# Kernel optimization log

Hardware: AMD Instinct MI355X
Metric: run time of the kernel (lower is better)

The kernel has to match this reference:

```python
import jax, jax.numpy as jnp
import numpy as np

MAX_STEPS = 12          # ns = ceil((t1-t0)/0.2) <= ceil(2/0.2) = 10 for unit dirs, unit sphere
BASE_STEP = 0.2
ABSORPTION = 0.1
SCATTERING = 0.1
DENSITY = 6.0
SIGMA = SCATTERING + ABSORPTION + 0.4   # 0.6, used in sample_transparency
BG = jnp.array([0.572, 0.772, 0.921], dtype=jnp.float32)
LIGHT_COLOR = jnp.array([1.3, 0.3, 0.9], dtype=jnp.float32)
RO = jnp.array([0.0, 0.0, 3.0], dtype=jnp.float32)   # hard-coded ray origin in original


def setup_inputs() -> dict:
    key = jax.random.key(0)
    W = H = 1024
    u = jnp.linspace(-0.5, 0.5, W, dtype=jnp.float32)
    v = jnp.linspace(-0.5, 0.5, H, dtype=jnp.float32)
    uu, vv = jnp.meshgrid(u, v, indexing='ij')
    d = jnp.stack([uu, vv, -jnp.ones_like(uu)], axis=-1)          # camera at z=3 looking at origin
    d = d + 0.001 * jax.random.normal(key, d.shape, dtype=jnp.float32)  # randn jitter
    dirs = d / jnp.linalg.norm(d, axis=-1, keepdims=True)          # unit directions -> bounded ns
    scene = jnp.array([[0.0, 0.0, 0.0, 1.0]], dtype=jnp.float32)   # unit sphere at origin
    return {"scene": scene, "dirs": dirs}


def _ray_march(scene, dirs):
    center = scene[0, 0:3]
    radius = scene[0, 3]
    rd = dirs                                      # [W,H,3]
    oc = RO - center                               # [3]
    a = jnp.sum(rd * rd, axis=-1)                  # [W,H]
    b = 2.0 * jnp.sum(rd * oc, axis=-1)
    c = jnp.dot(oc, oc) - radius * radius
    disc = b * b - 4.0 * a * c
    sq = jnp.sqrt(jnp.where(disc > 0, disc, 1.0))  # safe sqrt (masked later)
    x1 = (-b - sq) / (2.0 * a)
    x2 = (-b + sq) / (2.0 * a)
    # flag: disc>=0 and not (x1<0 and x2<0); since x1<=x2 this is x2>=0
    hit = (disc >= 0) & (x2 >= 0)                  # [W,H]
    t0 = jnp.maximum(x1, 0.0)                      # inside -> t0 = 0
    t1 = x2
    seg = t1 - t0
    ns = jnp.ceil(seg / BASE_STEP)                 # [W,H] float step count
    ns_safe = jnp.maximum(ns, 1.0)
    step = seg / ns_safe                           # per-pixel step size
    s = jnp.exp(-SIGMA * step)                     # per-step sample_transparency

    # static march over MAX_STEPS, masked by i < ns
    steps = jnp.arange(MAX_STEPS, dtype=jnp.float32)                 # [K]
    smask = (steps[None, None, :] < ns[..., None]) & hit[..., None]  # [W,H,K]
    t = t1[..., None] - (steps + 0.5) * step[..., None]              # [W,H,K]
    p = RO + t[..., None] * rd[..., None, :]                         # [W,H,K,3] sample points
    pc = p - center
    # light ray: origin p, direction (0,1,0) -> a=1
    lb = 2.0 * pc[..., 1]
    lc = jnp.sum(pc * pc, axis=-1) - radius * radius
    ld = lb * lb - 4.0 * lc
    lsq = jnp.sqrt(jnp.where(ld > 0, ld, 1.0))
    vt1 = (-lb + lsq) / 2.0
    lhit = (ld >= 0) & (vt1 >= 0)
    la = jnp.exp(-DENSITY * (SCATTERING + ABSORPTION) * vt1)         # light attenuation
    acc = jnp.sum(jnp.where(smask & lhit, la, 0.0), axis=-1)         # [W,H]

    # closed form of the original loop:
    #   result = sum_i la_i * light_color * s^(i+1) * scat*dens*step * s^(ns-i)
    #          = light_color * scat*dens*step * s^(ns+1) * sum_i la_i
    transparency = s ** ns
    result = (SCATTERING * DENSITY) * step * (s ** (ns + 1.0)) * acc  # [W,H]
    color_hit = BG * transparency[..., None] + LIGHT_COLOR * result[..., None]
    pixels = jnp.where(hit[..., None], color_hit, BG)                 # [W,H,3]
    return pixels


def reference(scene, dirs):
    return _ray_march(scene, dirs)
```

## Files before the change

kernel.cpp:

```cpp
#include <hip/hip_runtime.h>
#include <math.h>

__device__ __forceinline__ float fmulr(float a, float b) { return __fmul_rn(a, b); }
__device__ __forceinline__ float faddr(float a, float b) { return __fadd_rn(a, b); }
__device__ __forceinline__ float fsubr(float a, float b) { return __fsub_rn(a, b); }

struct Col { float x, y, z; };

__device__ __forceinline__ Col shade1(float rdx, float rdy, float rdz)
{
    const float BGx = 0.572f, BGy = 0.772f, BGz = 0.921f;
    Col out = {BGx, BGy, BGz};

    float a = faddr(faddr(fmulr(rdx, rdx), fmulr(rdy, rdy)), fmulr(rdz, rdz));
    float b = fmulr(2.0f, fmulr(rdz, 3.0f));
    float disc = fsubr(fmulr(b, b), fmulr(fmulr(4.0f, a), 8.0f));
    if (disc < 0.0f) return out;

    float sq = sqrtf(disc > 0.0f ? disc : 1.0f);
    float twoa = fmulr(2.0f, a);
    float x2 = faddr(-b, sq) / twoa;
    if (x2 < 0.0f) return out;
    float x1 = fsubr(-b, sq) / twoa;

    float t0 = fmaxf(x1, 0.0f);
    float t1 = x2;
    float seg = fsubr(t1, t0);
    float ns = ceilf(seg / 0.2f);
    float step = seg / fmaxf(ns, 1.0f);
    int nsi = (int)fminf(ns, 12.0f);

    float acc = 0.0f;
    for (int k = 0; k < nsi; ++k) {
        float t = fsubr(t1, fmulr((float)k + 0.5f, step));
        float pcx = fmulr(t, rdx);
        float pcy = fmulr(t, rdy);
        float pcz = faddr(3.0f, fmulr(t, rdz));
        float lb = fmulr(2.0f, pcy);
        float lc = fsubr(faddr(faddr(fmulr(pcx, pcx), fmulr(pcy, pcy)), fmulr(pcz, pcz)), 1.0f);
        float ld = fsubr(fmulr(lb, lb), fmulr(4.0f, lc));
        if (ld >= 0.0f) {
            float lsq = sqrtf(ld > 0.0f ? ld : 1.0f);
            float vt1 = fmulr(faddr(-lb, lsq), 0.5f);
            if (vt1 >= 0.0f) acc += __expf(-1.2f * vt1);
        }
    }

    float sn  = __expf(-0.6f * (step * ns));
    float sn1 = __expf(-0.6f * (step * (ns + 1.0f)));
    float result = 0.6f * step * sn1 * acc;
    out.x = BGx * sn + 1.3f * result;
    out.y = BGy * sn + 0.3f * result;
    out.z = BGz * sn + 0.9f * result;
    return out;
}

__device__ __forceinline__ Col shadeg(float rdx, float rdy, float rdz,
                                      float cx, float cy, float cz,
                                      float rr, float ocx, float ocy, float ocz,
                                      float cc)
{
    const float BGx = 0.572f, BGy = 0.772f, BGz = 0.921f;
    Col out = {BGx, BGy, BGz};

    float a = faddr(faddr(fmulr(rdx, rdx), fmulr(rdy, rdy)), fmulr(rdz, rdz));
    float b = fmulr(2.0f, faddr(faddr(fmulr(rdx, ocx), fmulr(rdy, ocy)), fmulr(rdz, ocz)));
    float disc = fsubr(fmulr(b, b), fmulr(fmulr(4.0f, a), cc));
    if (disc < 0.0f) return out;

    float sq = sqrtf(disc > 0.0f ? disc : 1.0f);
    float twoa = fmulr(2.0f, a);
    float x2 = faddr(-b, sq) / twoa;
    if (x2 < 0.0f) return out;
    float x1 = fsubr(-b, sq) / twoa;

    float t0 = fmaxf(x1, 0.0f);
    float t1 = x2;
    float seg = fsubr(t1, t0);
    float ns = ceilf(seg / 0.2f);
    float step = seg / fmaxf(ns, 1.0f);
    int nsi = (int)fminf(ns, 12.0f);

    float acc = 0.0f;
    for (int k = 0; k < nsi; ++k) {
        float t = fsubr(t1, fmulr((float)k + 0.5f, step));
        float pcx = fsubr(faddr(0.0f, fmulr(t, rdx)), cx);
        float pcy = fsubr(faddr(0.0f, fmulr(t, rdy)), cy);
        float pcz = fsubr(faddr(3.0f, fmulr(t, rdz)), cz);
        float lb = fmulr(2.0f, pcy);
        float lc = fsubr(faddr(faddr(fmulr(pcx, pcx), fmulr(pcy, pcy)), fmulr(pcz, pcz)), rr);
        float ld = fsubr(fmulr(lb, lb), fmulr(4.0f, lc));
        if (ld >= 0.0f) {
            float lsq = sqrtf(ld > 0.0f ? ld : 1.0f);
            float vt1 = fmulr(faddr(-lb, lsq), 0.5f);
            if (vt1 >= 0.0f) acc += __expf(-1.2f * vt1);
        }
    }

    float sn  = __expf(-0.6f * (step * ns));
    float sn1 = __expf(-0.6f * (step * (ns + 1.0f)));
    float result = 0.6f * step * sn1 * acc;
    out.x = BGx * sn + 1.3f * result;
    out.y = BGy * sn + 0.3f * result;
    out.z = BGz * sn + 0.9f * result;
    return out;
}

__global__ __launch_bounds__(256)
void raymarch_kernel(const float* __restrict__ scene,
                     const float* __restrict__ dirs,
                     float* __restrict__ out,
                     int npix)
{
    int p = blockIdx.x * blockDim.x + threadIdx.x;
    if (p >= npix) return;

    float rdx = dirs[3 * p + 0];
    float rdy = dirs[3 * p + 1];
    float rdz = dirs[3 * p + 2];

    float cx = scene[0], cy = scene[1], cz = scene[2], r = scene[3];

    Col c;
    if (cx == 0.0f && cy == 0.0f && cz == 0.0f && r == 1.0f) {
        c = shade1(rdx, rdy, rdz);
    } else {
        float rr = fmulr(r, r);
        float ocx = fsubr(0.0f, cx);
        float ocy = fsubr(0.0f, cy);
        float ocz = fsubr(3.0f, cz);
        float cc = fsubr(faddr(faddr(fmulr(ocx, ocx), fmulr(ocy, ocy)), fmulr(ocz, ocz)), rr);
        c = shadeg(rdx, rdy, rdz, cx, cy, cz, rr, ocx, ocy, ocz, cc);
    }

    out[3 * p + 0] = c.x;
    out[3 * p + 1] = c.y;
    out[3 * p + 2] = c.z;
}

extern "C" void kernel_launch(void* const* d_in, const int* in_sizes, int n_in,
                              void* d_out, int out_size, void* d_ws, size_t ws_size,
                              hipStream_t stream) {
    const float* scene = (const float*)d_in[0];
    const float* dirs  = (const float*)d_in[1];
    float* out = (float*)d_out;

    int npix = in_sizes[1] / 3;
    dim3 block(256);
    dim3 grid((npix + 255) / 256);
    raymarch_kernel<<<grid, block, 0, stream>>>(scene, dirs, out, npix);
}
```

Measured before the change: 72.78 us.

## Process four pixels per thread with float4 loads/stores and interleaved march

Each thread now shades four consecutive pixels, loading directions and storing colors with three float4 transactions instead of strided scalar accesses. The four rays' march loops are interleaved with predicated masking up to the maximum step count, giving instruction-level parallelism. Groups where no ray hits the sphere write the background directly. The general-scene path is made noinline to limit register pressure. In exchange, the kernel launches a quarter as many threads and spends wasted work on rays with fewer steps.

```diff
diff --git a/kernel.cpp b/kernel.cpp
--- a/kernel.cpp
+++ b/kernel.cpp
@@ -55,10 +55,10 @@
     return out;
 }
 
-__device__ __forceinline__ Col shadeg(float rdx, float rdy, float rdz,
-                                      float cx, float cy, float cz,
-                                      float rr, float ocx, float ocy, float ocz,
-                                      float cc)
+__device__ __noinline__ Col shadeg(float rdx, float rdy, float rdz,
+                                   float cx, float cy, float cz,
+                                   float rr, float ocx, float ocy, float ocz,
+                                   float cc)
 {
     const float BGx = 0.572f, BGy = 0.772f, BGz = 0.921f;
     Col out = {BGx, BGy, BGz};
@@ -107,35 +107,119 @@
 }
 
 __global__ __launch_bounds__(256)
-void raymarch_kernel(const float* __restrict__ scene,
-                     const float* __restrict__ dirs,
-                     float* __restrict__ out,
-                     int npix)
+void raymarch4_kernel(const float* __restrict__ scene,
+                      const float* __restrict__ dirs,
+                      float* __restrict__ out,
+                      int npix)
 {
-    int p = blockIdx.x * blockDim.x + threadIdx.x;
-    if (p >= npix) return;
-
-    float rdx = dirs[3 * p + 0];
-    float rdy = dirs[3 * p + 1];
-    float rdz = dirs[3 * p + 2];
+    const float BGx = 0.572f, BGy = 0.772f, BGz = 0.921f;
+
+    int t = blockIdx.x * blockDim.x + threadIdx.x;
+    int p0 = 4 * t;
+    if (p0 >= npix) return;
 
     float cx = scene[0], cy = scene[1], cz = scene[2], r = scene[3];
-
-    Col c;
-    if (cx == 0.0f && cy == 0.0f && cz == 0.0f && r == 1.0f) {
-        c = shade1(rdx, rdy, rdz);
-    } else {
-        float rr = fmulr(r, r);
-        float ocx = fsubr(0.0f, cx);
-        float ocy = fsubr(0.0f, cy);
-        float ocz = fsubr(3.0f, cz);
-        float cc = fsubr(faddr(faddr(fmulr(ocx, ocx), fmulr(ocy, ocy)), fmulr(ocz, ocz)), rr);
-        c = shadeg(rdx, rdy, rdz, cx, cy, cz, rr, ocx, ocy, ocz, cc);
-    }
-
-    out[3 * p + 0] = c.x;
-    out[3 * p + 1] = c.y;
-    out[3 * p + 2] = c.z;
+    bool special = (cx == 0.0f && cy == 0.0f && cz == 0.0f && r == 1.0f);
+
+    if (special && (p0 + 3 < npix)) {
+        const float4* d4 = (const float4*)dirs;
+        float4 A = d4[3 * t + 0];
+        float4 B = d4[3 * t + 1];
+        float4 C = d4[3 * t + 2];
+        float rdx[4] = {A.x, A.w, B.z, C.y};
+        float rdy[4] = {A.y, B.x, B.w, C.z};
+        float rdz[4] = {A.z, B.y, C.x, C.w};
+
+        float t1[4], stp[4], nsf[4], acc[4];
+        int nsi[4];
+        bool hit[4];
+
+        #pragma unroll
+        for (int j = 0; j < 4; ++j) {
+            float a = faddr(faddr(fmulr(rdx[j], rdx[j]), fmulr(rdy[j], rdy[j])), fmulr(rdz[j], rdz[j]));
+            float b = fmulr(2.0f, fmulr(rdz[j], 3.0f));
+            float disc = fsubr(fmulr(b, b), fmulr(fmulr(4.0f, a), 8.0f));
+            float sq = sqrtf(disc > 0.0f ? disc : 1.0f);
+            float twoa = fmulr(2.0f, a);
+            float x2 = faddr(-b, sq) / twoa;
+            float x1 = fsubr(-b, sq) / twoa;
+            bool h = (disc >= 0.0f) & (x2 >= 0.0f);
+            float t0 = fmaxf(x1, 0.0f);
+            float seg = fsubr(x2, t0);
+            float ns = ceilf(seg / 0.2f);
+            float st = seg / fmaxf(ns, 1.0f);
+            t1[j] = x2; stp[j] = st; nsf[j] = ns;
+            nsi[j] = h ? (int)fminf(ns, 12.0f) : 0;
+            hit[j] = h; acc[j] = 0.0f;
+        }
+
+        if (!(hit[0] | hit[1] | hit[2] | hit[3])) {
+            float4 O0 = {BGx, BGy, BGz, BGx};
+            float4 O1 = {BGy, BGz, BGx, BGy};
+            float4 O2 = {BGz, BGx, BGy, BGz};
+            float4* o4 = (float4*)out;
+            o4[3 * t + 0] = O0; o4[3 * t + 1] = O1; o4[3 * t + 2] = O2;
+            return;
+        }
+
+        int kmax = max(max(nsi[0], nsi[1]), max(nsi[2], nsi[3]));
+        for (int k = 0; k < kmax; ++k) {
+            float kf = faddr((float)k, 0.5f);
+            #pragma unroll
+            for (int j = 0; j < 4; ++j) {
+                float tt  = fsubr(t1[j], fmulr(kf, stp[j]));
+                float pcx = fmulr(tt, rdx[j]);
+                float pcy = fmulr(tt, rdy[j]);
+                float pcz = faddr(3.0f, fmulr(tt, rdz[j]));
+                float lb  = fmulr(2.0f, pcy);
+                float lc  = fsubr(faddr(faddr(fmulr(pcx, pcx), fmulr(pcy, pcy)), fmulr(pcz, pcz)), 1.0f);
+                float ld  = fsubr(fmulr(lb, lb), fmulr(4.0f, lc));
+                float lsq = sqrtf(ld > 0.0f ? ld : 1.0f);
+                float vt1 = fmulr(faddr(-lb, lsq), 0.5f);
+                bool act  = (k < nsi[j]) & (ld >= 0.0f) & (vt1 >= 0.0f);
+                acc[j] = faddr(acc[j], act ? __expf(-1.2f * vt1) : 0.0f);
+            }
+        }
+
+        float o[12];
+        #pragma unroll
+        for (int j = 0; j < 4; ++j) {
+            float sn  = __expf(-0.6f * (stp[j] * nsf[j]));
+            float sn1 = __expf(-0.6f * (stp[j] * (nsf[j] + 1.0f)));
+            float result = 0.6f * stp[j] * sn1 * acc[j];
+            float ox = BGx * sn + 1.3f * result;
+            float oy = BGy * sn + 0.3f * result;
+            float oz = BGz * sn + 0.9f * result;
+            o[3 * j + 0] = hit[j] ? ox : BGx;
+            o[3 * j + 1] = hit[j] ? oy : BGy;
+            o[3 * j + 2] = hit[j] ? oz : BGz;
+        }
+        float4 O0 = {o[0], o[1], o[2],  o[3]};
+        float4 O1 = {o[4], o[5], o[6],  o[7]};
+        float4 O2 = {o[8], o[9], o[10], o[11]};
+        float4* o4 = (float4*)out;
+        o4[3 * t + 0] = O0; o4[3 * t + 1] = O1; o4[3 * t + 2] = O2;
+        return;
+    }
+
+    float rr = fmulr(r, r);
+    float ocx = fsubr(0.0f, cx);
+    float ocy = fsubr(0.0f, cy);
+    float ocz = fsubr(3.0f, cz);
+    float cc = fsubr(faddr(faddr(fmulr(ocx, ocx), fmulr(ocy, ocy)), fmulr(ocz, ocz)), rr);
+
+    for (int j = 0; j < 4; ++j) {
+        int p = p0 + j;
+        if (p >= npix) break;
+        float rdx = dirs[3 * p + 0];
+        float rdy = dirs[3 * p + 1];
+        float rdz = dirs[3 * p + 2];
+        Col c = special ? shade1(rdx, rdy, rdz)
+                        : shadeg(rdx, rdy, rdz, cx, cy, cz, rr, ocx, ocy, ocz, cc);
+        out[3 * p + 0] = c.x;
+        out[3 * p + 1] = c.y;
+        out[3 * p + 2] = c.z;
+    }
 }
 
 extern "C" void kernel_launch(void* const* d_in, const int* in_sizes, int n_in,
@@ -146,7 +230,8 @@
     float* out = (float*)d_out;
 
     int npix = in_sizes[1] / 3;
+    int nthreads = (npix + 3) / 4;
     dim3 block(256);
-    dim3 grid((npix + 255) / 256);
-    raymarch_kernel<<<grid, block, 0, stream>>>(scene, dirs, out, npix);
-}
+    dim3 grid((nthreads + 255) / 256);
+    raymarch4_kernel<<<grid, block, 0, stream>>>(scene, dirs, out, npix);
+}
```

Result: slower. 75.23 us (+3.4%).
